# Performance work log

Hardware: AMD Instinct MI355X
Metric: run time of the kernel (lower is better)

The kernel has to match this reference:

```python
import jax, jax.numpy as jnp
import numpy as np

B, C, H, W = 8, 128, 128, 128
D_MODEL = C
D_INNER = 2 * D_MODEL          # expand=2 -> 256
D_STATE = 64
HEADDIM = 32                   # _resolve_headdim(128, 32) -> 32
NHEADS = D_INNER // HEADDIM    # 8
D_CONV = 4
CHUNK = 64
GN_GROUPS = 8                  # _group_count(128, 8)
D_XBC = D_INNER + 2 * D_STATE  # 384
D_INPROJ = 2 * D_INNER + 2 * D_STATE + NHEADS  # 648


def _group_norm(x, g, b, groups=GN_GROUPS, eps=1e-5):
    Bn, Cn, Hh, Ww = x.shape
    xr = x.reshape(Bn, groups, Cn // groups, Hh, Ww)
    mu = xr.mean(axis=(2, 3, 4), keepdims=True)
    var = xr.var(axis=(2, 3, 4), keepdims=True)
    xr = (xr - mu) * jax.lax.rsqrt(var + eps)
    return xr.reshape(Bn, Cn, Hh, Ww) * g[None, :, None, None] + b[None, :, None, None]


def _grid_sample_bilinear_border(img, grid):
    # img: (B,C,H,W); grid: (B,H,W,2) with (x,y) in [-1,1]; align_corners=True, border padding
    _, _, Hh, Ww = img.shape
    gx = jnp.clip((grid[..., 0] + 1.0) * 0.5 * (Ww - 1), 0.0, Ww - 1.0)
    gy = jnp.clip((grid[..., 1] + 1.0) * 0.5 * (Hh - 1), 0.0, Hh - 1.0)
    x0 = jnp.floor(gx); y0 = jnp.floor(gy)
    wx = gx - x0; wy = gy - y0
    x0i = x0.astype(jnp.int32); y0i = y0.astype(jnp.int32)
    x1i = jnp.minimum(x0i + 1, Ww - 1); y1i = jnp.minimum(y0i + 1, Hh - 1)
    def per_b(im, y0b, y1b, x0b, x1b, wxb, wyb):
        v00 = im[:, y0b, x0b]; v01 = im[:, y0b, x1b]
        v10 = im[:, y1b, x0b]; v11 = im[:, y1b, x1b]
        return (v00 * (1 - wxb) + v01 * wxb) * (1 - wyb) + (v10 * (1 - wxb) + v11 * wxb) * wyb
    return jax.vmap(per_b)(img, y0i, y1i, x0i, x1i, wx, wy)


def _mamba(seq, in_proj_w, conv_w, conv_b, dt_bias, A_log, D_skip, norm_g, out_w):
    # seq: (Bs, L, d_model) -> (Bs, L, d_model); Mamba2/SSD-style selective scan
    Bs, L, _ = seq.shape
    pad = (CHUNK - L % CHUNK) % CHUNK
    if pad:
        seq = jnp.pad(seq, ((0, 0), (0, pad), (0, 0)))
    Lp = L + pad
    zxbcdt = jnp.einsum('bld,ed->ble', seq, in_proj_w)
    z = zxbcdt[..., :D_INNER]
    xBC = zxbcdt[..., D_INNER:D_INNER + D_XBC]
    dt = jax.nn.softplus(zxbcdt[..., -NHEADS:] + dt_bias)  # (Bs,Lp,nh)
    # causal depthwise conv1d, kernel D_CONV
    xp = jnp.pad(xBC, ((0, 0), (D_CONV - 1, 0), (0, 0)))
    xBC = sum(conv_w[:, k] * xp[:, k:k + Lp, :] for k in range(D_CONV)) + conv_b
    xBC = jax.nn.silu(xBC)
    xs = xBC[..., :D_INNER].reshape(Bs, Lp, NHEADS, HEADDIM)
    Bm = xBC[..., D_INNER:D_INNER + D_STATE]
    Cm = xBC[..., D_INNER + D_STATE:]
    A = -jnp.exp(A_log)  # (nh,)
    def step(h, inp):
        x_t, B_t, C_t, dt_t = inp  # (Bs,nh,hd),(Bs,ds),(Bs,ds),(Bs,nh)
        dA = jnp.exp(dt_t * A)  # (Bs,nh)
        h = h * dA[..., None, None] + (dt_t[..., None] * x_t)[..., None] * B_t[:, None, None, :]
        y = jnp.einsum('bhds,bs->bhd', h, C_t)
        return h, y
    h0 = jnp.zeros((Bs, NHEADS, HEADDIM, D_STATE), seq.dtype)
    _, ys = jax.lax.scan(step, h0, (jnp.moveaxis(xs, 1, 0), jnp.moveaxis(Bm, 1, 0), jnp.moveaxis(Cm, 1, 0), jnp.moveaxis(dt, 1, 0)))
    ys = jnp.moveaxis(ys, 0, 1) + D_skip[None, None, :, None] * xs  # (Bs,Lp,nh,hd)
    y = ys.reshape(Bs, Lp, D_INNER) * jax.nn.silu(z)  # gated
    y = y * jax.lax.rsqrt(jnp.mean(y * y, axis=-1, keepdims=True) + 1e-5) * norm_g  # RMSNorm
    out = jnp.einsum('ble,de->bld', y, out_w)
    return out[:, :L] if pad else out


def _forward(x, dw_w, gn_g, gn_b, pw_w, pw_b, in_proj_w, conv_w, conv_b, dt_bias, A_log, D_skip, norm_g, out_w):
    Bn, Cn, Hh, Ww = x.shape
    dn = ('NCHW', 'OIHW', 'NCHW')
    # offset_net: depthwise 5x5 -> GroupNorm -> GELU -> 1x1
    h1 = jax.lax.conv_general_dilated(x, dw_w, (1, 1), 'SAME', feature_group_count=Cn, dimension_numbers=dn)
    h1 = jax.nn.gelu(_group_norm(h1, gn_g, gn_b), approximate=False)
    off = jax.lax.conv_general_dilated(h1, pw_w, (1, 1), 'SAME', dimension_numbers=dn) + pw_b[None, :, None, None]
    offset = jnp.tanh(off) * min(8.0, max(Hh, Ww) * 0.1)  # (B,1,H,W)
    gy = jnp.linspace(-1.0, 1.0, Hh, dtype=x.dtype)
    gx = jnp.linspace(-1.0, 1.0, Ww, dtype=x.dtype)
    base_y, base_x = jnp.meshgrid(gy, gx, indexing='ij')  # (H,W)
    off_n = offset[:, 0] * (2.0 / max(Hh - 1, 1))  # horizontal scan: vertical offsets
    grid = jnp.stack([jnp.broadcast_to(base_x, (Bn, Hh, Ww)), jnp.clip(base_y + off_n, -1.0, 1.0)], axis=-1)
    deformed = _grid_sample_bilinear_border(x, grid)
    seq = deformed.transpose(0, 2, 3, 1).reshape(Bn * Hh, Ww, Cn)  # (b h) w c
    out = _mamba(seq, in_proj_w, conv_w, conv_b, dt_bias, A_log, D_skip, norm_g, out_w)
    out_2d = out.reshape(Bn, Hh, Ww, Cn).transpose(0, 3, 1, 2)
    return out_2d, offset


def setup_inputs() -> dict:
    key = jax.random.key(0)
    ks = jax.random.split(key, 8)
    return {
        'x': jax.random.normal(ks[0], (B, C, H, W), jnp.float32),
        'dw_w': jax.random.normal(ks[1], (C, 1, 5, 5), jnp.float32) * 0.05,
        'gn_g': jnp.ones((C,), jnp.float32),
        'gn_b': jnp.zeros((C,), jnp.float32),
        'pw_w': jax.random.normal(ks[2], (1, C, 1, 1), jnp.float32) * 0.02,
        'pw_b': jnp.zeros((1,), jnp.float32),
        'in_proj_w': jax.random.normal(ks[3], (D_INPROJ, D_MODEL), jnp.float32) * 0.02,
        'conv_w': jax.random.normal(ks[4], (D_XBC, D_CONV), jnp.float32) * 0.1,
        'conv_b': jnp.zeros((D_XBC,), jnp.float32),
        'dt_bias': jax.random.normal(ks[5], (NHEADS,), jnp.float32) * 0.1,
        'A_log': jnp.log(jnp.arange(1, NHEADS + 1, dtype=jnp.float32)),
        'D_skip': jnp.ones((NHEADS,), jnp.float32),
        'norm_g': jnp.ones((D_INNER,), jnp.float32),
        'out_w': jax.random.normal(ks[6], (D_MODEL, D_INNER), jnp.float32) * 0.02,
    }


def reference(x, dw_w, gn_g, gn_b, pw_w, pw_b, in_proj_w, conv_w, conv_b, dt_bias, A_log, D_skip, norm_g, out_w):
    return _forward(x, dw_w, gn_g, gn_b, pw_w, pw_b, in_proj_w, conv_w, conv_b, dt_bias, A_log, D_skip, norm_g, out_w)
```

## Files before the change

kernel.cpp:

```cpp
#include <hip/hip_runtime.h>
#include <math.h>


typedef _Float16 half8 __attribute__((ext_vector_type(8)));
typedef _Float16 half4 __attribute__((ext_vector_type(4)));
typedef float f32x4 __attribute__((ext_vector_type(4)));

__device__ __forceinline__ float b2f(unsigned short u) {
  return __uint_as_float(((unsigned int)u) << 16);
}
__device__ __forceinline__ bool in_is_f32(const void* gng) {
  return ((const unsigned int*)gng)[0] == 0x3F800000u;
}

#define P_DWW 0
#define P_CW 3200
#define P_CB 4736
#define P_GNG 5120
#define P_GNB 5248
#define P_PWW 5376
#define P_PWB 5504
#define P_DTB 5505
#define P_ALOG 5513
#define P_DSKIP 5521
#define P_NG 5529

__global__ void k_prep_all(const void* dww, const void* cw, const void* cb,
                           const void* gng, const void* gnb, const void* pww,
                           const void* pwb, const void* dtbias, const void* alog,
                           const void* dskip, const void* ng,
                           const void* wproj, const void* outw,
                           float* __restrict__ P, float* __restrict__ gst,
                           _Float16* __restrict__ wprojh, _Float16* __restrict__ outwh) {
  bool f = in_is_f32(gng);
  int stride = gridDim.x * blockDim.x;
  for (int i = blockIdx.x * blockDim.x + threadIdx.x; i < 98304; i += stride) {
    int row = i >> 7;
    float v = 0.f;
    if (row < 648) v = f ? ((const float*)wproj)[i] : b2f(((const unsigned short*)wproj)[i]);
    wprojh[i] = (_Float16)v;
  }
  for (int i = blockIdx.x * blockDim.x + threadIdx.x; i < 32768; i += stride) {
    int e = i & 255;
    float wv = f ? ((const float*)outw)[i] : b2f(((const unsigned short*)outw)[i]);
    float ngv = f ? ((const float*)ng)[e] : b2f(((const unsigned short*)ng)[e]);
    outwh[i] = (_Float16)(wv * ngv);
  }
  if (blockIdx.x == 0) {
    int tid = threadIdx.x;
    if (tid < 128) gst[tid] = 0.f;
    auto cvt = [&](const void* src, int n, int off) {
      for (int i = tid; i < n; i += 256)
        P[off + i] = f ? ((const float*)src)[i] : b2f(((const unsigned short*)src)[i]);
    };
    cvt(dww, 3200, P_DWW);
    cvt(cw, 1536, P_CW);
    cvt(cb, 384, P_CB);
    cvt(gng, 128, P_GNG);
    cvt(gnb, 128, P_GNB);
    cvt(pww, 128, P_PWW);
    cvt(pwb, 1, P_PWB);
    cvt(dtbias, 8, P_DTB);
    cvt(alog, 8, P_ALOG);
    cvt(dskip, 8, P_DSKIP);
    cvt(ng, 256, P_NG);
  }
}

__global__ __launch_bounds__(256) void k_dwconv_v6(const void* __restrict__ x,
                                                   const void* __restrict__ gng,
                                                   const float* __restrict__ P,
                                                   _Float16* __restrict__ h1h,
                                                   float* __restrict__ gst) {
  int bc = blockIdx.x;
  int b = bc >> 7, c = bc & 127;
  bool f32x = in_is_f32(gng);
  __shared__ float red[8];
  const float* xf = (const float*)x + (size_t)bc * 16384;
  const unsigned short* xb = (const unsigned short*)x + (size_t)bc * 16384;
  float w[25];
#pragma unroll
  for (int k = 0; k < 25; ++k) w[k] = P[P_DWW + c * 25 + k];

  int ox = (threadIdx.x & 31) * 4;
  int y0 = (threadIdx.x >> 5) * 16;
  float win[5][12];

  auto loadrow = [&](int gy, float* d) {
#pragma unroll
    for (int k = 0; k < 12; ++k) d[k] = 0.f;
    if (gy >= 0 && gy < 128) {
      if (f32x) {
        const float* rp = xf + gy * 128;
        if (ox >= 4) {
          float4 v = *(const float4*)(rp + ox - 4);
          d[0] = v.x; d[1] = v.y; d[2] = v.z; d[3] = v.w;
        }
        float4 v0 = *(const float4*)(rp + ox);
        d[4] = v0.x; d[5] = v0.y; d[6] = v0.z; d[7] = v0.w;
        if (ox < 124) {
          float4 v1 = *(const float4*)(rp + ox + 4);
          d[8] = v1.x; d[9] = v1.y; d[10] = v1.z; d[11] = v1.w;
        }
      } else {
        const unsigned short* rp = xb + gy * 128;
        if (ox >= 4) {
          ushort4 u = *(const ushort4*)(rp + ox - 4);
          d[0] = b2f(u.x); d[1] = b2f(u.y); d[2] = b2f(u.z); d[3] = b2f(u.w);
        }
        ushort4 u0 = *(const ushort4*)(rp + ox);
        d[4] = b2f(u0.x); d[5] = b2f(u0.y); d[6] = b2f(u0.z); d[7] = b2f(u0.w);
        if (ox < 124) {
          ushort4 u1 = *(const ushort4*)(rp + ox + 4);
          d[8] = b2f(u1.x); d[9] = b2f(u1.y); d[10] = b2f(u1.z); d[11] = b2f(u1.w);
        }
      }
    }
  };

#pragma unroll
  for (int i = 0; i < 4; ++i) loadrow(y0 - 2 + i, win[i]);

  float s = 0.f, sq = 0.f;
  _Float16* hp = h1h + (size_t)bc * 16384;
#pragma unroll
  for (int yo = 0; yo < 16; ++yo) {
    loadrow(y0 + yo + 2, win[(yo + 4) % 5]);
    float o4[4] = {0.f, 0.f, 0.f, 0.f};
#pragma unroll
    for (int ky = 0; ky < 5; ++ky) {
      const float* r = win[(yo + ky) % 5];
#pragma unroll
      for (int j = 0; j < 4; ++j)
#pragma unroll
        for (int kx = 0; kx < 5; ++kx)
          o4[j] += w[ky * 5 + kx] * r[j + kx + 2];
    }
    half4 oh;
#pragma unroll
    for (int j = 0; j < 4; ++j) {
      oh[j] = (_Float16)o4[j];
      s += o4[j]; sq += o4[j] * o4[j];
    }
    *(half4*)&hp[(y0 + yo) * 128 + ox] = oh;
  }

  for (int o = 32; o; o >>= 1) { s += __shfl_down(s, o, 64); sq += __shfl_down(sq, o, 64); }
  int wv = threadIdx.x >> 6;
  if ((threadIdx.x & 63) == 0) { red[wv] = s; red[4 + wv] = sq; }
  __syncthreads();
  if (threadIdx.x == 0) {
    float ts = red[0] + red[1] + red[2] + red[3];
    float tq = red[4] + red[5] + red[6] + red[7];
    int g = (b << 3) + (c >> 4);
    atomicAdd(&gst[g * 2], ts);
    atomicAdd(&gst[g * 2 + 1], tq);
  }
}

__global__ __launch_bounds__(256) void k_gn_part(const _Float16* __restrict__ h1h,
                                                 const float* __restrict__ gst,
                                                 const float* __restrict__ P,
                                                 float* __restrict__ part) {
  int bh2 = blockIdx.x;
  int b = bh2 >> 8;
  int h = (bh2 & 255) >> 1;
  int half = bh2 & 1;
  int tid = threadIdx.x;
  int w = tid & 127;
  int sub = tid >> 7;
  __shared__ float ls[8];
  __shared__ float sacc[2][128];
  if (tid < 4) {
    const float invN = 1.f / 262144.f;
    int g = b * 8 + half * 4 + tid;
    float mean = gst[g * 2] * invN;
    float var = gst[g * 2 + 1] * invN - mean * mean;
    ls[tid * 2] = mean;
    ls[tid * 2 + 1] = rsqrtf(var + 1e-5f);
  }
  __syncthreads();
  int cbase = half * 64 + sub * 32;
  const _Float16* hb = h1h + (((size_t)(b * 128 + cbase)) * 128 + h) * 128 + w;
  float acc = 0.f;
#pragma unroll 4
  for (int ci = 0; ci < 32; ++ci) {
    int c = cbase + ci;
    float v = (float)hb[(size_t)ci * 16384];
    int lg = (sub * 32 + ci) >> 4;
    float nv = (v - ls[lg * 2]) * ls[lg * 2 + 1] * P[P_GNG + c] + P[P_GNB + c];
    float ge = 0.5f * nv * (1.f + erff(nv * 0.70710678118f));
    acc += ge * P[P_PWW + c];
  }
  sacc[sub][w] = acc;
  __syncthreads();
  if (sub == 0) part[(size_t)bh2 * 128 + w] = acc + sacc[1][w];
}

__global__ __launch_bounds__(256) void k_deform_v5(const void* __restrict__ x,
                                                   const void* __restrict__ gng,
                                                   const float* __restrict__ part,
                                                   const float* __restrict__ P,
                                                   _Float16* __restrict__ seqc,
                                                   float* __restrict__ dout,
                                                   int s0) {
  int bh = s0 + blockIdx.x;
  int b = bh >> 7, h = bh & 127;
  int tid = threadIdx.x;
  int w = tid & 127;
  int half = tid >> 7;
  bool f32x = in_is_f32(gng);
  __shared__ float t[128 * 129];
  float ofv = tanhf(part[(size_t)bh * 256 + w] + part[(size_t)bh * 256 + 128 + w] +
                    P[P_PWB]) * 8.0f;
  if (half == 0) dout[16777216 + bh * 128 + w] = ofv;
  float gy = -1.f + (2.f / 127.f) * (float)h + ofv * (2.f / 127.f);
  gy = fminf(fmaxf(gy, -1.f), 1.f);
  float py = (gy + 1.f) * 0.5f * 127.f;
  py = fminf(fmaxf(py, 0.f), 127.f);
  float y0f = floorf(py);
  float wy = py - y0f;
  int y0 = (int)y0f;
  int y1 = min(y0 + 1, 127);
  const float* xfb = (const float*)x + (size_t)b * 128 * 16384;
  const unsigned short* xbb = (const unsigned short*)x + (size_t)b * 128 * 16384;
  int c0 = half * 64;
  for (int i = 0; i < 64; i += 2) {
    int ca = c0 + i, cb2 = c0 + i + 1;
    size_t a0 = (size_t)ca * 16384 + y0 * 128 + w;
    size_t a1 = (size_t)ca * 16384 + y1 * 128 + w;
    size_t b0 = (size_t)cb2 * 16384 + y0 * 128 + w;
    size_t b1 = (size_t)cb2 * 16384 + y1 * 128 + w;
    float va0, va1, vb0, vb1;
    if (f32x) { va0 = xfb[a0]; va1 = xfb[a1]; vb0 = xfb[b0]; vb1 = xfb[b1]; }
    else      { va0 = b2f(xbb[a0]); va1 = b2f(xbb[a1]);
                vb0 = b2f(xbb[b0]); vb1 = b2f(xbb[b1]); }
    t[ca * 129 + w] = va0 + wy * (va1 - va0);
    t[cb2 * 129 + w] = vb0 + wy * (vb1 - vb0);
  }
  __syncthreads();
  int c2 = tid & 127;
  int lb = (tid >> 7) * 64;
  _Float16* sp = seqc + (size_t)blockIdx.x * 16384;
  for (int i = 0; i < 64; ++i) {
    int l = lb + i;
    sp[l * 128 + c2] = (_Float16)t[c2 * 129 + l];
  }
}

__global__ __launch_bounds__(256) void k_gemm1_v7(const _Float16* __restrict__ seqh,
                                                  const _Float16* __restrict__ wprojh,
                                                  const float* __restrict__ P,
                                                  _Float16* __restrict__ zh,
                                                  _Float16* __restrict__ xch,
                                                  float* __restrict__ dtb) {
  __shared__ __align__(16) _Float16 lds[16896];
  _Float16* lA = lds;
  _Float16* lB = lds + 8192;
  int m0 = blockIdx.x * 128;
  int e0 = blockIdx.y * 128;
  int tid = threadIdx.x;
  int lane = tid & 63;
  int wv = tid >> 6;
  f32x4 acc[2][8];
#pragma unroll
  for (int rf = 0; rf < 2; ++rf)
#pragma unroll
    for (int cf = 0; cf < 8; ++cf) acc[rf][cf] = (f32x4){0.f, 0.f, 0.f, 0.f};

  int rsel = lane & 15, q = lane >> 4;
  for (int k0 = 0; k0 < 128; k0 += 64) {
    if (k0) __syncthreads();
#pragma unroll
    for (int p = 0; p < 4; ++p) {
      int idx = tid + 256 * p;
      int row = idx >> 3, ch = idx & 7;
      int dch = ch ^ (row & 7);
      *(half8*)&lA[row * 64 + dch * 8] =
          *(const half8*)&seqh[(size_t)(m0 + row) * 128 + k0 + ch * 8];
      *(half8*)&lB[row * 64 + dch * 8] =
          *(const half8*)&wprojh[(size_t)(e0 + row) * 128 + k0 + ch * 8];
    }
    __syncthreads();
#pragma unroll
    for (int kk = 0; kk < 2; ++kk) {
      half8 a[2];
#pragma unroll
      for (int rf = 0; rf < 2; ++rf) {
        int row = wv * 32 + rf * 16 + rsel;
        int ch = (kk * 4 + q) ^ (row & 7);
        a[rf] = *(const half8*)&lA[row * 64 + ch * 8];
      }
#pragma unroll
      for (int cf = 0; cf < 8; ++cf) {
        int row = cf * 16 + rsel;
        int ch = (kk * 4 + q) ^ (row & 7);
        half8 b = *(const half8*)&lB[row * 64 + ch * 8];
        acc[0][cf] = __builtin_amdgcn_mfma_f32_16x16x32_f16(a[0], b, acc[0][cf], 0, 0, 0);
        acc[1][cf] = __builtin_amdgcn_mfma_f32_16x16x32_f16(a[1], b, acc[1][cf], 0, 0, 0);
      }
    }
  }

  if (e0 < 256) {
#pragma unroll
    for (int rf = 0; rf < 2; ++rf) {
      int mb = m0 + wv * 32 + rf * 16 + q * 4;
#pragma unroll
      for (int cf = 0; cf < 8; ++cf) {
        _Float16* pz = zh + (size_t)mb * 256 + e0 + cf * 16 + rsel;
#pragma unroll
        for (int r = 0; r < 4; ++r) pz[(size_t)r * 256] = (_Float16)acc[rf][cf][r];
      }
    }
  } else if (e0 < 640) {
    __syncthreads();
#pragma unroll
    for (int rf = 0; rf < 2; ++rf) {
#pragma unroll
      for (int r = 0; r < 4; ++r) {
        int row = wv * 32 + rf * 16 + q * 4 + r;
#pragma unroll
        for (int cf = 0; cf < 8; ++cf)
          lds[row * 132 + cf * 16 + rsel] = (_Float16)acc[rf][cf][r];
      }
    }
    __syncthreads();
    int cc = tid & 127;
    int rh = tid >> 7;
    int eg = (e0 - 256) + cc;
    float w0 = P[P_CW + eg * 4 + 0], w1 = P[P_CW + eg * 4 + 1];
    float w2 = P[P_CW + eg * 4 + 2], w3 = P[P_CW + eg * 4 + 3];
    float bb = P[P_CB + eg];
    int r0 = rh * 64;
    float x0 = (r0 >= 3) ? (float)lds[(r0 - 3) * 132 + cc] : 0.f;
    float x1 = (r0 >= 2) ? (float)lds[(r0 - 2) * 132 + cc] : 0.f;
    float x2 = (r0 >= 1) ? (float)lds[(r0 - 1) * 132 + cc] : 0.f;
    _Float16* xo = xch + (size_t)m0 * 384 + eg;
    for (int r = r0; r < r0 + 64; ++r) {
      float x3 = (float)lds[r * 132 + cc];
      float a = bb + w0 * x0 + w1 * x1 + w2 * x2 + w3 * x3;
      xo[(size_t)r * 384] = (_Float16)(a / (1.f + __expf(-a)));
      x0 = x1; x1 = x2; x2 = x3;
    }
  } else {
#pragma unroll
    for (int rf = 0; rf < 2; ++rf) {
      int mb = m0 + wv * 32 + rf * 16 + q * 4;
      if (rsel < 8) {
        float bias = P[P_DTB + rsel];
#pragma unroll
        for (int r = 0; r < 4; ++r) {
          float dv = acc[rf][0][r] + bias;
          float sp = (dv > 20.f) ? dv : log1pf(__expf(dv));
          dtb[(size_t)(mb + r) * 8 + rsel] = sp;
        }
      }
    }
  }
}

__global__ __launch_bounds__(256) void k_ssd_v2(const _Float16* __restrict__ xch,
                                                const _Float16* __restrict__ zh,
                                                const float* __restrict__ dtb,
                                                const float* __restrict__ P,
                                                _Float16* __restrict__ ys,
                                                float* __restrict__ rr) {
  int seq = blockIdx.x;
  int tid = threadIdx.x;
  int lane = tid & 63, wv = tid >> 6;
  int rsel = lane & 15, q = lane >> 4;
  __shared__ __align__(16) _Float16 G[128 * 128];
  __shared__ __align__(16) _Float16 Xt[32 * 128];
  __shared__ float dts[128 * 8];
  __shared__ float Ts[8 * 128];
  const _Float16* xb = xch + (size_t)seq * 49152;
  const _Float16* zb = zh + (size_t)seq * 32768;
  const float* dtp = dtb + (size_t)seq * 1024;

  for (int i = tid; i < 1024; i += 256) dts[i] = dtp[i];
  __syncthreads();
  if (tid < 8) {
    float a = 0.f;
    for (int l = 0; l < 128; ++l) { a += dts[l * 8 + tid]; Ts[tid * 128 + l] = a; }
  }

  f32x4 gacc[2][8];
#pragma unroll
  for (int rf = 0; rf < 2; ++rf)
#pragma unroll
    for (int cf = 0; cf < 8; ++cf) gacc[rf][cf] = (f32x4){0.f, 0.f, 0.f, 0.f};
#pragma unroll
  for (int kk = 0; kk < 2; ++kk) {
    half8 a[2];
#pragma unroll
    for (int rf = 0; rf < 2; ++rf) {
      int l = wv * 32 + rf * 16 + rsel;
      a[rf] = *(const half8*)&xb[(size_t)l * 384 + 320 + kk * 32 + q * 8];
    }
#pragma unroll
    for (int cf = 0; cf < 8; ++cf) {
      int j = cf * 16 + rsel;
      half8 b = *(const half8*)&xb[(size_t)j * 384 + 256 + kk * 32 + q * 8];
      gacc[0][cf] = __builtin_amdgcn_mfma_f32_16x16x32_f16(a[0], b, gacc[0][cf], 0, 0, 0);
      gacc[1][cf] = __builtin_amdgcn_mfma_f32_16x16x32_f16(a[1], b, gacc[1][cf], 0, 0, 0);
    }
  }
#pragma unroll
  for (int rf = 0; rf < 2; ++rf) {
#pragma unroll
    for (int r = 0; r < 4; ++r) {
      int l = wv * 32 + rf * 16 + q * 4 + r;
#pragma unroll
      for (int cf = 0; cf < 8; ++cf) {
        int j = cf * 16 + rsel;
        G[l * 128 + (((j >> 3) ^ (l & 7)) << 3) + (j & 7)] = (_Float16)gacc[rf][cf][r];
      }
    }
  }
  __syncthreads();

  float ssq[2][4];
#pragma unroll
  for (int rf = 0; rf < 2; ++rf)
#pragma unroll
    for (int r = 0; r < 4; ++r) ssq[rf][r] = 0.f;

  _Float16* yp = ys + (size_t)seq * 32768;
  for (int h = 0; h < 8; ++h) {
    {
      int j = tid >> 1, ds = (tid & 1) * 16;
      float dtj = dts[j * 8 + h];
      half8 v0 = *(const half8*)&xb[(size_t)j * 384 + h * 32 + ds];
      half8 v1 = *(const half8*)&xb[(size_t)j * 384 + h * 32 + ds + 8];
#pragma unroll
      for (int e = 0; e < 8; ++e) {
        int d0 = ds + e, d1 = ds + 8 + e;
        Xt[d0 * 128 + (((j >> 3) ^ (d0 & 7)) << 3) + (j & 7)] = (_Float16)((float)v0[e] * dtj);
        Xt[d1 * 128 + (((j >> 3) ^ (d1 & 7)) << 3) + (j & 7)] = (_Float16)((float)v1[e] * dtj);
      }
    }
    __syncthreads();
    float Ah = -__expf(P[P_ALOG + h]);
    float Dk = P[P_DSKIP + h];
    f32x4 acc[2][2];
#pragma unroll
    for (int rf = 0; rf < 2; ++rf)
#pragma unroll
      for (int cf = 0; cf < 2; ++cf) acc[rf][cf] = (f32x4){0.f, 0.f, 0.f, 0.f};
#pragma unroll
    for (int kk = 0; kk < 4; ++kk) {
      int jb = kk * 32 + q * 8;
      int chk = kk * 4 + q;
      float4 tj0 = *(const float4*)&Ts[h * 128 + jb];
      float4 tj1 = *(const float4*)&Ts[h * 128 + jb + 4];
      float tj[8] = {tj0.x, tj0.y, tj0.z, tj0.w, tj1.x, tj1.y, tj1.z, tj1.w};
      half8 a[2];
#pragma unroll
      for (int rf = 0; rf < 2; ++rf) {
        int l = wv * 32 + rf * 16 + rsel;
        half8 g = *(const half8*)&G[l * 128 + ((chk ^ (l & 7)) << 3)];
        float Tl = Ts[h * 128 + l];
        half8 w;
#pragma unroll
        for (int e = 0; e < 8; ++e) {
          int j = jb + e;
          float m = (j <= l) ? __expf(Ah * (Tl - tj[e])) : 0.f;
          w[e] = (_Float16)((float)g[e] * m);
        }
        a[rf] = w;
      }
#pragma unroll
      for (int cf = 0; cf < 2; ++cf) {
        int d = cf * 16 + rsel;
        half8 b = *(const half8*)&Xt[d * 128 + ((chk ^ (d & 7)) << 3)];
        acc[0][cf] = __builtin_amdgcn_mfma_f32_16x16x32_f16(a[0], b, acc[0][cf], 0, 0, 0);
        acc[1][cf] = __builtin_amdgcn_mfma_f32_16x16x32_f16(a[1], b, acc[1][cf], 0, 0, 0);
      }
    }
#pragma unroll
    for (int rf = 0; rf < 2; ++rf) {
      int lb = wv * 32 + rf * 16 + q * 4;
#pragma unroll
      for (int cf = 0; cf < 2; ++cf) {
        int d = cf * 16 + rsel;
#pragma unroll
        for (int r = 0; r < 4; ++r) {
          int l = lb + r;
          float xv = (float)xb[(size_t)l * 384 + h * 32 + d];
          float zv = (float)zb[(size_t)l * 256 + h * 32 + d];
          float y = acc[rf][cf][r] + Dk * xv;
          float yg = y * (zv / (1.f + __expf(-zv)));
          ssq[rf][r] += yg * yg;
          yp[(size_t)l * 256 + h * 32 + d] = (_Float16)yg;
        }
      }
    }
    __syncthreads();
  }

  float* rp = rr + (size_t)seq * 128;
#pragma unroll
  for (int rf = 0; rf < 2; ++rf) {
#pragma unroll
    for (int r = 0; r < 4; ++r) {
      float ss = ssq[rf][r];
      ss += __shfl_xor(ss, 1, 64);
      ss += __shfl_xor(ss, 2, 64);
      ss += __shfl_xor(ss, 4, 64);
      ss += __shfl_xor(ss, 8, 64);
      if (rsel == 0) rp[wv * 32 + rf * 16 + q * 4 + r] = rsqrtf(ss * (1.f / 256.f) + 1e-5f);
    }
  }
}

__global__ __launch_bounds__(256) void k_gemm2_v4(const _Float16* __restrict__ ysg,
                                                  const float* __restrict__ rr,
                                                  const _Float16* __restrict__ outwh,
                                                  float* __restrict__ dout,
                                                  int tok0) {
  __shared__ __align__(16) _Float16 lA[128 * 64];
  __shared__ __align__(16) _Float16 lB[64 * 64];
  int t0 = blockIdx.x * 64;
  int tid = threadIdx.x;
  int lane = tid & 63;
  int wv = tid >> 6;
  f32x4 acc[2][4];
#pragma unroll
  for (int rf = 0; rf < 2; ++rf)
#pragma unroll
    for (int cf = 0; cf < 4; ++cf) acc[rf][cf] = (f32x4){0.f, 0.f, 0.f, 0.f};

  int rsel = lane & 15, q = lane >> 4;
  for (int k0 = 0; k0 < 256; k0 += 64) {
    if (k0) __syncthreads();
#pragma unroll
    for (int p = 0; p < 4; ++p) {
      int idx = tid + 256 * p;
      int row = idx >> 3, ch = idx & 7;
      int dch = ch ^ (row & 7);
      *(half8*)&lA[row * 64 + dch * 8] =
          *(const half8*)&outwh[(size_t)row * 256 + k0 + ch * 8];
    }
#pragma unroll
    for (int p = 0; p < 2; ++p) {
      int idx = tid + 256 * p;
      int row = idx >> 3, ch = idx & 7;
      int dch = ch ^ (row & 7);
      float rv = rr[t0 + row];
      half8 v = *(const half8*)&ysg[(size_t)(t0 + row) * 256 + k0 + ch * 8];
      half8 o;
#pragma unroll
      for (int e = 0; e < 8; ++e) o[e] = (_Float16)((float)v[e] * rv);
      *(half8*)&lB[row * 64 + dch * 8] = o;
    }
    __syncthreads();
#pragma unroll
    for (int kk = 0; kk < 2; ++kk) {
      half8 a[2];
#pragma unroll
      for (int rf = 0; rf < 2; ++rf) {
        int row = wv * 32 + rf * 16 + rsel;
        int ch = (kk * 4 + q) ^ (row & 7);
        a[rf] = *(const half8*)&lA[row * 64 + ch * 8];
      }
#pragma unroll
      for (int cf = 0; cf < 4; ++cf) {
        int row = cf * 16 + rsel;
        int ch = (kk * 4 + q) ^ (row & 7);
        half8 b = *(const half8*)&lB[row * 64 + ch * 8];
        acc[0][cf] = __builtin_amdgcn_mfma_f32_16x16x32_f16(a[0], b, acc[0][cf], 0, 0, 0);
        acc[1][cf] = __builtin_amdgcn_mfma_f32_16x16x32_f16(a[1], b, acc[1][cf], 0, 0, 0);
      }
    }
  }

  int l0 = tok0 + t0;
  int b = l0 >> 14;
  int rem0 = l0 & 16383;
#pragma unroll
  for (int rf = 0; rf < 2; ++rf) {
    int cbase = wv * 32 + rf * 16 + q * 4;
#pragma unroll
    for (int cf = 0; cf < 4; ++cf) {
#pragma unroll
      for (int r = 0; r < 4; ++r) {
        dout[(size_t)(b * 128 + cbase + r) * 16384 + rem0 + cf * 16 + rsel] = acc[rf][cf][r];
      }
    }
  }
}

extern "C" void kernel_launch(void* const* d_in, const int* in_sizes, int n_in,
                              void* d_out, int out_size, void* d_ws, size_t ws_size,
                              hipStream_t stream) {
  const void* x      = d_in[0];
  const void* dww    = d_in[1];
  const void* gng    = d_in[2];
  const void* gnb    = d_in[3];
  const void* pww    = d_in[4];
  const void* pwb    = d_in[5];
  const void* wproj  = d_in[6];
  const void* cw     = d_in[7];
  const void* cb     = d_in[8];
  const void* dtbias = d_in[9];
  const void* alog   = d_in[10];
  const void* dskip  = d_in[11];
  const void* ng     = d_in[12];
  const void* outw   = d_in[13];
  float* out = (float*)d_out;

  char* ws = (char*)d_ws;
  float* gst        = (float*)(ws + 0);
  float* P          = (float*)(ws + 8192);
  _Float16* wprojh  = (_Float16*)(ws + 40960);
  _Float16* outwh   = (_Float16*)(ws + 372736);
  float* part       = (float*)(ws + 503808);
  char* cbase       = ws + 1552384;

  _Float16* h1h = (_Float16*)out;

  const int opts[11] = {1024, 512, 256, 128, 64, 32, 16, 8, 4, 2, 1};
  int CH = 1;
  for (int i = 0; i < 11; ++i) {
    if (1552384ull + (unsigned long long)opts[i] * 266752ull <= (unsigned long long)ws_size) {
      CH = opts[i];
      break;
    }
  }
  int NC = 1024 / CH;

  _Float16* seqh = (_Float16*)(cbase);
  _Float16* zh   = (_Float16*)(cbase + (size_t)CH * 32768);
  _Float16* xch  = (_Float16*)(cbase + (size_t)CH * 98304);
  float* dtbf    = (float*)(cbase + (size_t)CH * 196608);
  _Float16* ysh  = (_Float16*)(cbase + (size_t)CH * 200704);
  float* rrf     = (float*)(cbase + (size_t)CH * 266240);

  k_prep_all<<<128, 256, 0, stream>>>(dww, cw, cb, gng, gnb, pww, pwb, dtbias,
                                      alog, dskip, ng, wproj, outw, P, gst,
                                      wprojh, outwh);
  k_dwconv_v6<<<1024, 256, 0, stream>>>(x, gng, P, h1h, gst);
  k_gn_part<<<2048, 256, 0, stream>>>(h1h, gst, P, part);

  int M = CH * 128;
  for (int c = 0; c < NC; ++c) {
    int s0 = c * CH;
    k_deform_v5<<<CH, 256, 0, stream>>>(x, gng, part, P, seqh, out, s0);
    k_gemm1_v7<<<dim3(M / 128, 6), 256, 0, stream>>>(seqh, wprojh, P, zh, xch, dtbf);
    k_ssd_v2<<<CH, 256, 0, stream>>>(xch, zh, dtbf, P, ysh, rrf);
    k_gemm2_v4<<<dim3(M / 64), 256, 0, stream>>>(ysh, rrf, outwh, out, s0 * 128);
  }
}
```

Before: 469.1 us.

## Split SSD kernel across two head groups and defer RMS-norm reduction

The SSD kernel now launches a second grid dimension so each block handles four of the eight heads, doubling the number of blocks. Because the RMS norm needs the sum of squares over all heads, each half writes partial sums and the output GEMM kernel adds the two partials and applies rsqrt. The intent is higher occupancy and parallelism in the SSD stage. The cost is that each block still recomputes the full C·B^T Gram matrix and reloads dt, so that work is done twice.

```diff
diff --git a/kernel.cpp b/kernel.cpp
--- a/kernel.cpp
+++ b/kernel.cpp
@@ -360,29 +360,31 @@
   }
 }
 
-__global__ __launch_bounds__(256) void k_ssd_v2(const _Float16* __restrict__ xch,
+__global__ __launch_bounds__(256) void k_ssd_v3(const _Float16* __restrict__ xch,
                                                 const _Float16* __restrict__ zh,
                                                 const float* __restrict__ dtb,
                                                 const float* __restrict__ P,
                                                 _Float16* __restrict__ ys,
-                                                float* __restrict__ rr) {
+                                                float* __restrict__ ssqp) {
   int seq = blockIdx.x;
+  int hb = blockIdx.y;
   int tid = threadIdx.x;
   int lane = tid & 63, wv = tid >> 6;
   int rsel = lane & 15, q = lane >> 4;
   __shared__ __align__(16) _Float16 G[128 * 128];
   __shared__ __align__(16) _Float16 Xt[32 * 128];
   __shared__ float dts[128 * 8];
-  __shared__ float Ts[8 * 128];
+  __shared__ float Ts[4 * 128];
   const _Float16* xb = xch + (size_t)seq * 49152;
   const _Float16* zb = zh + (size_t)seq * 32768;
   const float* dtp = dtb + (size_t)seq * 1024;
 
   for (int i = tid; i < 1024; i += 256) dts[i] = dtp[i];
   __syncthreads();
-  if (tid < 8) {
+  if (tid < 4) {
+    int h = hb * 4 + tid;
     float a = 0.f;
-    for (int l = 0; l < 128; ++l) { a += dts[l * 8 + tid]; Ts[tid * 128 + l] = a; }
+    for (int l = 0; l < 128; ++l) { a += dts[l * 8 + h]; Ts[tid * 128 + l] = a; }
   }
 
   f32x4 gacc[2][8];
@@ -427,7 +429,8 @@
     for (int r = 0; r < 4; ++r) ssq[rf][r] = 0.f;
 
   _Float16* yp = ys + (size_t)seq * 32768;
-  for (int h = 0; h < 8; ++h) {
+  for (int hh = 0; hh < 4; ++hh) {
+    int h = hb * 4 + hh;
     {
       int j = tid >> 1, ds = (tid & 1) * 16;
       float dtj = dts[j * 8 + h];
@@ -452,15 +455,15 @@
     for (int kk = 0; kk < 4; ++kk) {
       int jb = kk * 32 + q * 8;
       int chk = kk * 4 + q;
-      float4 tj0 = *(const float4*)&Ts[h * 128 + jb];
-      float4 tj1 = *(const float4*)&Ts[h * 128 + jb + 4];
+      float4 tj0 = *(const float4*)&Ts[hh * 128 + jb];
+      float4 tj1 = *(const float4*)&Ts[hh * 128 + jb + 4];
       float tj[8] = {tj0.x, tj0.y, tj0.z, tj0.w, tj1.x, tj1.y, tj1.z, tj1.w};
       half8 a[2];
 #pragma unroll
       for (int rf = 0; rf < 2; ++rf) {
         int l = wv * 32 + rf * 16 + rsel;
         half8 g = *(const half8*)&G[l * 128 + ((chk ^ (l & 7)) << 3)];
-        float Tl = Ts[h * 128 + l];
+        float Tl = Ts[hh * 128 + l];
         half8 w;
 #pragma unroll
         for (int e = 0; e < 8; ++e) {
@@ -499,7 +502,7 @@
     __syncthreads();
   }
 
-  float* rp = rr + (size_t)seq * 128;
+  float* rp = ssqp + ((size_t)hb * gridDim.x + seq) * 128;
 #pragma unroll
   for (int rf = 0; rf < 2; ++rf) {
 #pragma unroll
@@ -509,13 +512,14 @@
       ss += __shfl_xor(ss, 2, 64);
       ss += __shfl_xor(ss, 4, 64);
       ss += __shfl_xor(ss, 8, 64);
-      if (rsel == 0) rp[wv * 32 + rf * 16 + q * 4 + r] = rsqrtf(ss * (1.f / 256.f) + 1e-5f);
-    }
-  }
-}
-
-__global__ __launch_bounds__(256) void k_gemm2_v4(const _Float16* __restrict__ ysg,
-                                                  const float* __restrict__ rr,
+      if (rsel == 0) rp[wv * 32 + rf * 16 + q * 4 + r] = ss;
+    }
+  }
+}
+
+__global__ __launch_bounds__(256) void k_gemm2_v5(const _Float16* __restrict__ ysg,
+                                                  const float* __restrict__ ssqA,
+                                                  const float* __restrict__ ssqB,
                                                   const _Float16* __restrict__ outwh,
                                                   float* __restrict__ dout,
                                                   int tok0) {
@@ -547,7 +551,8 @@
       int idx = tid + 256 * p;
       int row = idx >> 3, ch = idx & 7;
       int dch = ch ^ (row & 7);
-      float rv = rr[t0 + row];
+      float ss = ssqA[t0 + row] + ssqB[t0 + row];
+      float rv = rsqrtf(ss * (1.f / 256.f) + 1e-5f);
       half8 v = *(const half8*)&ysg[(size_t)(t0 + row) * 256 + k0 + ch * 8];
       half8 o;
 #pragma unroll
@@ -623,7 +628,7 @@
   const int opts[11] = {1024, 512, 256, 128, 64, 32, 16, 8, 4, 2, 1};
   int CH = 1;
   for (int i = 0; i < 11; ++i) {
-    if (1552384ull + (unsigned long long)opts[i] * 266752ull <= (unsigned long long)ws_size) {
+    if (1552384ull + (unsigned long long)opts[i] * 267264ull <= (unsigned long long)ws_size) {
       CH = opts[i];
       break;
     }
@@ -635,7 +640,7 @@
   _Float16* xch  = (_Float16*)(cbase + (size_t)CH * 98304);
   float* dtbf    = (float*)(cbase + (size_t)CH * 196608);
   _Float16* ysh  = (_Float16*)(cbase + (size_t)CH * 200704);
-  float* rrf     = (float*)(cbase + (size_t)CH * 266240);
+  float* ssqp    = (float*)(cbase + (size_t)CH * 266240);
 
   k_prep_all<<<128, 256, 0, stream>>>(dww, cw, cb, gng, gnb, pww, pwb, dtbias,
                                       alog, dskip, ng, wproj, outw, P, gst,
@@ -644,11 +649,13 @@
   k_gn_part<<<2048, 256, 0, stream>>>(h1h, gst, P, part);
 
   int M = CH * 128;
+  float* ssqA = ssqp;
+  float* ssqB = ssqp + (size_t)CH * 128;
   for (int c = 0; c < NC; ++c) {
     int s0 = c * CH;
     k_deform_v5<<<CH, 256, 0, stream>>>(x, gng, part, P, seqh, out, s0);
     k_gemm1_v7<<<dim3(M / 128, 6), 256, 0, stream>>>(seqh, wprojh, P, zh, xch, dtbf);
-    k_ssd_v2<<<CH, 256, 0, stream>>>(xch, zh, dtbf, P, ysh, rrf);
-    k_gemm2_v4<<<dim3(M / 64), 256, 0, stream>>>(ysh, rrf, outwh, out, s0 * 128);
-  }
-}
+    k_ssd_v3<<<dim3(CH, 2), 256, 0, stream>>>(xch, zh, dtbf, P, ysh, ssqp);
+    k_gemm2_v5<<<dim3(M / 64), 256, 0, stream>>>(ysh, ssqA, ssqB, outwh, out, s0 * 128);
+  }
+}
```

After: 500.0 us. 1.07x slower.
